# Optimization experiments

Measured on AMD Instinct MI355X. Metric: run time of the kernel, lower is better.

Reference implementation:

```python
import jax, jax.numpy as jnp
import numpy as np

B, X, H = 2048, 1024, 1024
DR = 0.5

def setup_inputs() -> dict:
    key = jax.random.key(0)
    ks = jax.random.split(key, 21)
    std = 1.0 / np.sqrt(H)
    u = lambda k, s: jax.random.uniform(k, s, jnp.float32, -std, std)
    bern = lambda k, s: (jax.random.bernoulli(k, 1.0 - DR, s) / (1.0 - DR)).astype(jnp.float32)
    return {
        "x": jax.random.normal(ks[0], (B, X), jnp.float32),
        "h0": jax.random.normal(ks[1], (B, H), jnp.float32),
        "c0": jax.random.normal(ks[2], (B, H), jnp.float32),
        "w_xi": u(ks[3], (H, X)), "w_xf": u(ks[4], (H, X)),
        "w_xc": u(ks[5], (H, X)), "w_xo": u(ks[6], (H, X)),
        "w_hi": u(ks[7], (H, H)), "w_hf": u(ks[8], (H, H)),
        "w_hc": u(ks[9], (H, H)), "w_ho": u(ks[10], (H, H)),
        "b_i": u(ks[11], (H,)), "b_f": u(ks[12], (H,)),
        "b_c": u(ks[13], (H,)), "b_o": u(ks[14], (H,)),
        "maskHI": bern(ks[15], (B, H)), "maskHF": bern(ks[16], (B, H)),
        "maskHC": bern(ks[17], (B, H)), "maskHO": bern(ks[18], (B, H)),
        "maskC": bern(ks[19], (B, H)),
    }

def reference(x, h0, c0,
              w_xi, w_xf, w_xc, w_xo,
              w_hi, w_hf, w_hc, w_ho,
              b_i, b_f, b_c, b_o,
              maskHI, maskHF, maskHC, maskHO, maskC):
    # gal dropout: per-gate masks on recurrent input h0
    hs = jnp.stack([h0 * maskHI, h0 * maskHF, h0 * maskHC, h0 * maskHO])  # [4,B,H]
    wh = jnp.stack([w_hi, w_hf, w_hc, w_ho])                              # [4,H,H]
    wx = jnp.stack([w_xi, w_xf, w_xc, w_xo])                              # [4,H,X]
    # two batched GEMMs (F.linear uses x @ W.T)
    g = jnp.einsum('bx,gkx->gbk', x, wx) + jnp.einsum('gbh,gkh->gbk', hs, wh)
    gateI = jax.nn.sigmoid(g[0] + b_i)
    gateF = jax.nn.sigmoid(g[1] + b_f)
    gateC = jnp.tanh(g[2] + b_c) * maskC   # sem dropout on candidate
    gateO = jax.nn.sigmoid(g[3] + b_o)
    c1 = gateF * c0 + gateI * gateC
    h1 = gateO * jnp.tanh(c1)
    return (h1, c1)
```

## Files before the change

### kernel.cpp

```cpp
#include <hip/hip_runtime.h>
#include <hip/hip_bf16.h>
#include <stdint.h>

#define BDIM 2048
#define HDIM 1024
#define XDIM 1024
#define BH (BDIM*HDIM)
#define WSEG 1048576

typedef __attribute__((ext_vector_type(8))) short short8;
typedef __attribute__((ext_vector_type(4))) float float4v;

__device__ __forceinline__ void gload16(const void* g, void* l) {
    __builtin_amdgcn_global_load_lds(
        (const __attribute__((address_space(1))) unsigned int*)g,
        (__attribute__((address_space(3))) unsigned int*)l, 16, 0, 0);
}

__device__ __forceinline__ unsigned pack2(float a, float b) {
    __hip_bfloat162 v = __float22bfloat162_rn(make_float2(a, b));
    return *reinterpret_cast<unsigned*>(&v);
}
__device__ __forceinline__ uint2 pack4(float4 f) {
    return make_uint2(pack2(f.x, f.y), pack2(f.z, f.w));
}
__device__ __forceinline__ float2 up2(unsigned u) {
    __hip_bfloat162 v = *reinterpret_cast<__hip_bfloat162*>(&u);
    return __bfloat1622float2(v);
}

__global__ __launch_bounds__(256) void prep_all_k(
    const float* __restrict__ w0, const float* __restrict__ w1,
    const float* __restrict__ w2, const float* __restrict__ w3,
    const float* __restrict__ w4, const float* __restrict__ w5,
    const float* __restrict__ w6, const float* __restrict__ w7,
    const float* __restrict__ x, const float* __restrict__ h0,
    const float* __restrict__ mI, const float* __restrict__ mF,
    const float* __restrict__ mC, const float* __restrict__ mO,
    uint2* __restrict__ dst) {
    const int seg = blockIdx.y;
    const int i = blockIdx.x * 256 + threadIdx.x;
    float4 f;
    if (seg < 10) {
        const float* base;
        switch (seg) {
            case 0: base = w0; break; case 1: base = w1; break;
            case 2: base = w2; break; case 3: base = w3; break;
            case 4: base = w4; break; case 5: base = w5; break;
            case 6: base = w6; break; case 7: base = w7; break;
            default: base = x + (size_t)(seg - 8) * WSEG; break;
        }
        f = ((const float4*)base)[i];
    } else {
        const int s = seg - 10;
        const int g = s >> 1, half = s & 1;
        const float* mp = (g == 0) ? mI : (g == 1) ? mF : (g == 2) ? mC : mO;
        float4 h = ((const float4*)(h0 + (size_t)half * WSEG))[i];
        float4 m = ((const float4*)(mp + (size_t)half * WSEG))[i];
        f = make_float4(h.x * m.x, h.y * m.y, h.z * m.z, h.w * m.w);
    }
    dst[(size_t)seg * (WSEG / 4) + i] = pack4(f);
}

__global__ __launch_bounds__(256, 4) void gemm_split(
    const __hip_bfloat16* __restrict__ ws18,
    __hip_bfloat16* __restrict__ part) {
    const int id = blockIdx.x;
    const int z = id & 7;
    const int by = (id >> 3) & 7;
    const int bx = id >> 6;
    const int g = z >> 1, half = z & 1;
    const __hip_bfloat16* Ap = half ? (ws18 + (size_t)(10 + 2 * g) * WSEG)
                                    : (ws18 + (size_t)8 * WSEG);
    const __hip_bfloat16* Bp = half ? (ws18 + (size_t)(4 + g) * WSEG)
                                    : (ws18 + (size_t)g * WSEG);

    __shared__ __hip_bfloat16 As[128 * 64];
    __shared__ __hip_bfloat16 Bs[128 * 64];

    const int t = threadIdx.x;
    const int m0 = bx * 128;
    const int n0 = by * 128;
    const int wv = t >> 6, lane = t & 63;
    const int wm = (wv >> 1) * 64, wn = (wv & 1) * 64;
    const int quad = lane >> 4, lrow = lane & 15;

    float4v acc[4][4];
#pragma unroll
    for (int i = 0; i < 4; ++i)
#pragma unroll
        for (int j = 0; j < 4; ++j) acc[i][j] = (float4v){0.f, 0.f, 0.f, 0.f};

    const short8* As8 = (const short8*)As;
    const short8* Bs8 = (const short8*)Bs;

    for (int k0 = 0; k0 < 1024; k0 += 64) {
#pragma unroll
        for (int it = 0; it < 4; ++it) {
            int chunk = it * 256 + t;
            int row = chunk >> 3;
            int ccs = (chunk & 7) ^ (row & 7);
            gload16(Ap + (size_t)(m0 + row) * 1024 + k0 + ccs * 8,
                    (char*)As + chunk * 16);
            gload16(Bp + (size_t)(n0 + row) * 1024 + k0 + ccs * 8,
                    (char*)Bs + chunk * 16);
        }
        __syncthreads();

#pragma unroll
        for (int ks = 0; ks < 2; ++ks) {
            short8 af[4], bfr[4];
#pragma unroll
            for (int mt = 0; mt < 4; ++mt) {
                int r = wm + mt * 16 + lrow;
                af[mt] = As8[(r << 3) + ((ks * 4 + quad) ^ (r & 7))];
            }
#pragma unroll
            for (int nt = 0; nt < 4; ++nt) {
                int r = wn + nt * 16 + lrow;
                bfr[nt] = Bs8[(r << 3) + ((ks * 4 + quad) ^ (r & 7))];
            }
#pragma unroll
            for (int mt = 0; mt < 4; ++mt)
#pragma unroll
                for (int nt = 0; nt < 4; ++nt)
                    acc[mt][nt] = __builtin_amdgcn_mfma_f32_16x16x32_bf16(
                        af[mt], bfr[nt], acc[mt][nt], 0, 0, 0);
        }
        __syncthreads();
    }

    __hip_bfloat16* pz = part + (size_t)z * BH;
#pragma unroll
    for (int nt = 0; nt < 4; ++nt) {
        int col = n0 + wn + nt * 16 + lrow;
#pragma unroll
        for (int mt = 0; mt < 4; ++mt) {
#pragma unroll
            for (int r = 0; r < 4; ++r) {
                int row = m0 + wm + mt * 16 + quad * 4 + r;
                pz[(size_t)row * HDIM + col] = __float2bfloat16(acc[mt][nt][r]);
            }
        }
    }
}

__global__ __launch_bounds__(256) void combine_k(
    const uint2* __restrict__ part,
    const float* __restrict__ bi, const float* __restrict__ bff,
    const float* __restrict__ bc, const float* __restrict__ bo,
    const float* __restrict__ c0, const float* __restrict__ mC,
    float4* __restrict__ out) {
    const int i = blockIdx.x * 256 + threadIdx.x;
    const int h4 = (i * 4 & (HDIM - 1)) >> 2;

    float gate[4][4];
#pragma unroll
    for (int g = 0; g < 4; ++g) {
        uint2 p0 = part[(size_t)(2 * g) * (BH / 4) + i];
        uint2 p1 = part[(size_t)(2 * g + 1) * (BH / 4) + i];
        float2 a0 = up2(p0.x), a1 = up2(p0.y);
        float2 b0 = up2(p1.x), b1 = up2(p1.y);
        gate[g][0] = a0.x + b0.x;
        gate[g][1] = a0.y + b0.y;
        gate[g][2] = a1.x + b1.x;
        gate[g][3] = a1.y + b1.y;
    }
    float4 vbi = ((const float4*)bi)[h4];
    float4 vbf = ((const float4*)bff)[h4];
    float4 vbc = ((const float4*)bc)[h4];
    float4 vbo = ((const float4*)bo)[h4];
    float4 vc0 = ((const float4*)c0)[i];
    float4 vmc = ((const float4*)mC)[i];
    const float* pbi = (const float*)&vbi;
    const float* pbf = (const float*)&vbf;
    const float* pbc = (const float*)&vbc;
    const float* pbo = (const float*)&vbo;
    const float* pc0 = (const float*)&vc0;
    const float* pmc = (const float*)&vmc;

    float h1[4], c1[4];
#pragma unroll
    for (int j = 0; j < 4; ++j) {
        float xi = gate[0][j] + pbi[j];
        float xf = gate[1][j] + pbf[j];
        float xc = gate[2][j] + pbc[j];
        float xo = gate[3][j] + pbo[j];
        float I = 1.f / (1.f + __expf(-xi));
        float F = 1.f / (1.f + __expf(-xf));
        float C = tanhf(xc) * pmc[j];
        float O = 1.f / (1.f + __expf(-xo));
        c1[j] = F * pc0[j] + I * C;
        h1[j] = O * tanhf(c1[j]);
    }
    out[i] = make_float4(h1[0], h1[1], h1[2], h1[3]);
    out[BH / 4 + i] = make_float4(c1[0], c1[1], c1[2], c1[3]);
}

extern "C" void kernel_launch(void* const* d_in, const int* in_sizes, int n_in,
                              void* d_out, int out_size, void* d_ws, size_t ws_size,
                              hipStream_t stream) {
    const float* x   = (const float*)d_in[0];
    const float* h0  = (const float*)d_in[1];
    const float* c0  = (const float*)d_in[2];
    const float* wxi = (const float*)d_in[3];
    const float* wxf = (const float*)d_in[4];
    const float* wxc = (const float*)d_in[5];
    const float* wxo = (const float*)d_in[6];
    const float* whi = (const float*)d_in[7];
    const float* whf = (const float*)d_in[8];
    const float* whc = (const float*)d_in[9];
    const float* who = (const float*)d_in[10];
    const float* bi  = (const float*)d_in[11];
    const float* bf  = (const float*)d_in[12];
    const float* bc  = (const float*)d_in[13];
    const float* bo  = (const float*)d_in[14];
    const float* mI  = (const float*)d_in[15];
    const float* mF  = (const float*)d_in[16];
    const float* mC  = (const float*)d_in[17];
    const float* mO  = (const float*)d_in[18];
    const float* mCell = (const float*)d_in[19];

    __hip_bfloat16* ws18 = (__hip_bfloat16*)d_ws;
    __hip_bfloat16* part = ws18 + (size_t)18 * WSEG;

    prep_all_k<<<dim3(WSEG / 4 / 256, 18), dim3(256), 0, stream>>>(
        wxi, wxf, wxc, wxo, whi, whf, whc, who, x, h0, mI, mF, mC, mO,
        (uint2*)ws18);

    gemm_split<<<dim3(1024), dim3(256), 0, stream>>>(ws18, part);

    combine_k<<<dim3(BH / 4 / 256), dim3(256), 0, stream>>>(
        (const uint2*)part, bi, bf, bc, bo, c0, mCell, (float4*)d_out);
}
```

Measured before the change: 202.9 us.

## Rewrite GEMM as 256x256-tile double-buffered pipeline with interleaved loads and MFMA

The split GEMM moves from 128x128 tiles with 256 threads and a single LDS buffer to 256x256 tiles with 512 threads (8 waves, each computing 128x64). LDS is double-buffered at 128 KB, and global-to-LDS loads for the next k-tile are issued in quarter slices between MFMA groups. Raw s_barrier, explicit vmcnt waits and setprio hints are used to overlap memory traffic with compute. This aims to raise operand reuse and hide load latency, at the cost of only 256 blocks on the device and much higher register and LDS pressure per block.

Result: no change. 200.6 us (-1.1%).

```diff
diff --git a/kernel.cpp b/kernel.cpp
--- a/kernel.cpp
+++ b/kernel.cpp
@@ -62,85 +62,177 @@
     dst[(size_t)seg * (WSEG / 4) + i] = pack4(f);
 }
 
-__global__ __launch_bounds__(256, 4) void gemm_split(
+
+#define BARRIER() asm volatile("s_barrier" ::: "memory")
+
+__device__ __forceinline__ void stage_half(const __hip_bfloat16* __restrict__ gp,
+                                           short* lb, int t) {
+    const int r0 = t >> 3;
+    const int c0 = (t & 7) ^ (r0 & 7);
+    gload16(gp + (size_t)r0 * 1024 + c0 * 8, (char*)lb + t * 16);
+    const int r1 = r0 + 64;
+    const int c1 = (t & 7) ^ (r1 & 7);
+    gload16(gp + (size_t)r1 * 1024 + c1 * 8, (char*)lb + t * 16 + 8192);
+}
+
+template<int P>
+__device__ __forceinline__ void read_bf(const short8* L8, int wn_i, int lrow, int quad,
+                                        short8 (&bfr)[4][2]) {
+    const int bb8 = 4096 + P * 2048 + (wn_i >> 1) * 1024;
+#pragma unroll
+    for (int nt = 0; nt < 4; ++nt) {
+        const int rb = (wn_i & 1) * 64 + nt * 16 + lrow;
+#pragma unroll
+        for (int ks = 0; ks < 2; ++ks)
+            bfr[nt][ks] = L8[bb8 + (rb << 3) + ((ks * 4 + quad) ^ (rb & 7))];
+    }
+}
+
+template<int P, int Q>
+__device__ __forceinline__ void read_af(const short8* L8, int wm_i, int lrow, int quad,
+                                        short8 (&af)[2][2]) {
+    const int ab8 = P * 2048 + wm_i * 1024;
+#pragma unroll
+    for (int sub = 0; sub < 2; ++sub) {
+        const int ra = Q * 32 + sub * 16 + lrow;
+#pragma unroll
+        for (int ks = 0; ks < 2; ++ks)
+            af[sub][ks] = L8[ab8 + (ra << 3) + ((ks * 4 + quad) ^ (ra & 7))];
+    }
+}
+
+template<int Q>
+__device__ __forceinline__ void mfma_q(short8 (&af)[2][2], short8 (&bfr)[4][2],
+                                       float4v (&acc)[8][4]) {
+    __builtin_amdgcn_s_setprio(1);
+#pragma unroll
+    for (int sub = 0; sub < 2; ++sub)
+#pragma unroll
+        for (int nt = 0; nt < 4; ++nt)
+#pragma unroll
+            for (int ks = 0; ks < 2; ++ks)
+                acc[2 * Q + sub][nt] = __builtin_amdgcn_mfma_f32_16x16x32_bf16(
+                    af[sub][ks], bfr[nt][ks], acc[2 * Q + sub][nt], 0, 0, 0);
+    __builtin_amdgcn_s_setprio(0);
+}
+
+__global__ __launch_bounds__(512, 2) void gemm_split(
     const __hip_bfloat16* __restrict__ ws18,
     __hip_bfloat16* __restrict__ part) {
     const int id = blockIdx.x;
     const int z = id & 7;
-    const int by = (id >> 3) & 7;
-    const int bx = id >> 6;
+    const int w = id >> 3;
+    const int by = w & 3;
+    const int bx = w >> 2;
     const int g = z >> 1, half = z & 1;
     const __hip_bfloat16* Ap = half ? (ws18 + (size_t)(10 + 2 * g) * WSEG)
                                     : (ws18 + (size_t)8 * WSEG);
     const __hip_bfloat16* Bp = half ? (ws18 + (size_t)(4 + g) * WSEG)
                                     : (ws18 + (size_t)g * WSEG);
 
-    __shared__ __hip_bfloat16 As[128 * 64];
-    __shared__ __hip_bfloat16 Bs[128 * 64];
+    __shared__ short lds[65536];
 
     const int t = threadIdx.x;
-    const int m0 = bx * 128;
-    const int n0 = by * 128;
-    const int wv = t >> 6, lane = t & 63;
-    const int wm = (wv >> 1) * 64, wn = (wv & 1) * 64;
-    const int quad = lane >> 4, lrow = lane & 15;
-
-    float4v acc[4][4];
-#pragma unroll
-    for (int i = 0; i < 4; ++i)
+    const int m0 = bx * 256, n0 = by * 256;
+    const int wid = t >> 6, lane = t & 63;
+    const int wm_i = wid >> 2, wn_i = wid & 3;
+    const int lrow = lane & 15, quad = lane >> 4;
+    const short8* L8 = (const short8*)lds;
+
+    float4v acc[8][4];
+#pragma unroll
+    for (int i = 0; i < 8; ++i)
 #pragma unroll
         for (int j = 0; j < 4; ++j) acc[i][j] = (float4v){0.f, 0.f, 0.f, 0.f};
 
-    const short8* As8 = (const short8*)As;
-    const short8* Bs8 = (const short8*)Bs;
-
-    for (int k0 = 0; k0 < 1024; k0 += 64) {
-#pragma unroll
-        for (int it = 0; it < 4; ++it) {
-            int chunk = it * 256 + t;
-            int row = chunk >> 3;
-            int ccs = (chunk & 7) ^ (row & 7);
-            gload16(Ap + (size_t)(m0 + row) * 1024 + k0 + ccs * 8,
-                    (char*)As + chunk * 16);
-            gload16(Bp + (size_t)(n0 + row) * 1024 + k0 + ccs * 8,
-                    (char*)Bs + chunk * 16);
+    auto stageA = [&](int k, int h) {
+        stage_half(Ap + (size_t)(m0 + h * 128) * 1024 + (size_t)k * 64,
+                   lds + (k & 1) * 16384 + h * 8192, t);
+    };
+    auto stageB = [&](int k, int h) {
+        stage_half(Bp + (size_t)(n0 + h * 128) * 1024 + (size_t)k * 64,
+                   lds + 32768 + (k & 1) * 16384 + h * 8192, t);
+    };
+
+    stageA(0, 0); stageA(0, 1); stageB(0, 0); stageB(0, 1); stageB(1, 0); stageB(1, 1);
+    asm volatile("s_waitcnt vmcnt(4)" ::: "memory");
+    BARRIER();
+
+    auto iter_body = [&](int i, bool last) {
+        const int T1 = 2 * i + 1;
+        short8 bfr[4][2];
+        short8 af[2][2];
+
+        read_bf<0>(L8, wn_i, lrow, quad, bfr);
+        read_af<0, 0>(L8, wm_i, lrow, quad, af);
+        stageA(T1, 0);
+        BARRIER(); __builtin_amdgcn_sched_barrier(0);
+        mfma_q<0>(af, bfr, acc);
+        BARRIER();
+
+        read_af<0, 1>(L8, wm_i, lrow, quad, af);
+        stageA(T1, 1);
+        BARRIER(); __builtin_amdgcn_sched_barrier(0);
+        mfma_q<1>(af, bfr, acc);
+        BARRIER();
+
+        read_af<0, 2>(L8, wm_i, lrow, quad, af);
+        if (!last) stageB(T1 + 1, 0);
+        BARRIER(); __builtin_amdgcn_sched_barrier(0);
+        mfma_q<2>(af, bfr, acc);
+        BARRIER();
+
+        read_af<0, 3>(L8, wm_i, lrow, quad, af);
+        if (!last) stageB(T1 + 1, 1);
+        BARRIER(); __builtin_amdgcn_sched_barrier(0);
+        mfma_q<3>(af, bfr, acc);
+        if (last) asm volatile("s_waitcnt vmcnt(0)" ::: "memory");
+        else      asm volatile("s_waitcnt vmcnt(4)" ::: "memory");
+        BARRIER();
+
+        read_bf<1>(L8, wn_i, lrow, quad, bfr);
+        read_af<1, 0>(L8, wm_i, lrow, quad, af);
+        if (!last) stageA(T1 + 1, 0);
+        BARRIER(); __builtin_amdgcn_sched_barrier(0);
+        mfma_q<0>(af, bfr, acc);
+        BARRIER();
+
+        read_af<1, 1>(L8, wm_i, lrow, quad, af);
+        if (!last) stageA(T1 + 1, 1);
+        BARRIER(); __builtin_amdgcn_sched_barrier(0);
+        mfma_q<1>(af, bfr, acc);
+        BARRIER();
+
+        read_af<1, 2>(L8, wm_i, lrow, quad, af);
+        if (!last) stageB(T1 + 2, 0);
+        BARRIER(); __builtin_amdgcn_sched_barrier(0);
+        mfma_q<2>(af, bfr, acc);
+        BARRIER();
+
+        read_af<1, 3>(L8, wm_i, lrow, quad, af);
+        if (!last) stageB(T1 + 2, 1);
+        BARRIER(); __builtin_amdgcn_sched_barrier(0);
+        mfma_q<3>(af, bfr, acc);
+        if (!last) {
+            asm volatile("s_waitcnt vmcnt(4)" ::: "memory");
+            BARRIER();
         }
-        __syncthreads();
-
-#pragma unroll
-        for (int ks = 0; ks < 2; ++ks) {
-            short8 af[4], bfr[4];
-#pragma unroll
-            for (int mt = 0; mt < 4; ++mt) {
-                int r = wm + mt * 16 + lrow;
-                af[mt] = As8[(r << 3) + ((ks * 4 + quad) ^ (r & 7))];
-            }
-#pragma unroll
-            for (int nt = 0; nt < 4; ++nt) {
-                int r = wn + nt * 16 + lrow;
-                bfr[nt] = Bs8[(r << 3) + ((ks * 4 + quad) ^ (r & 7))];
-            }
-#pragma unroll
-            for (int mt = 0; mt < 4; ++mt)
-#pragma unroll
-                for (int nt = 0; nt < 4; ++nt)
-                    acc[mt][nt] = __builtin_amdgcn_mfma_f32_16x16x32_bf16(
-                        af[mt], bfr[nt], acc[mt][nt], 0, 0, 0);
-        }
-        __syncthreads();
-    }
+    };
+
+#pragma unroll 1
+    for (int i = 0; i < 7; ++i) iter_body(i, false);
+    iter_body(7, true);
 
     __hip_bfloat16* pz = part + (size_t)z * BH;
 #pragma unroll
-    for (int nt = 0; nt < 4; ++nt) {
-        int col = n0 + wn + nt * 16 + lrow;
-#pragma unroll
-        for (int mt = 0; mt < 4; ++mt) {
-#pragma unroll
-            for (int r = 0; r < 4; ++r) {
-                int row = m0 + wm + mt * 16 + quad * 4 + r;
-                pz[(size_t)row * HDIM + col] = __float2bfloat16(acc[mt][nt][r]);
-            }
+    for (int mt = 0; mt < 8; ++mt) {
+        const int rowb = m0 + wm_i * 128 + mt * 16 + quad * 4;
+#pragma unroll
+        for (int nt = 0; nt < 4; ++nt) {
+            const int col = n0 + wn_i * 64 + nt * 16 + lrow;
+#pragma unroll
+            for (int r = 0; r < 4; ++r)
+                pz[(size_t)(rowb + r) * HDIM + col] = __float2bfloat16(acc[mt][nt][r]);
         }
     }
 }
@@ -228,7 +320,7 @@
         wxi, wxf, wxc, wxo, whi, whf, whc, who, x, h0, mI, mF, mC, mO,
         (uint2*)ws18);
 
-    gemm_split<<<dim3(1024), dim3(256), 0, stream>>>(ws18, part);
+    gemm_split<<<dim3(256), dim3(512), 0, stream>>>(ws18, part);
 
     combine_k<<<dim3(BH / 4 / 256), dim3(256), 0, stream>>>(
         (const uint2*)part, bi, bf, bc, bo, c0, mCell, (float4*)d_out);
```

## Enlarge GEMM tiles to 256x256 with double-buffered LDS prefetch

Applied to the files above, without the earlier changes.

The split GEMM now uses 512-thread blocks computing 256x256 output tiles, with each wave holding a 128x64 sub-tile. It double-buffers the 64-wide K slices in 128 KB of LDS, issuing the next slice's global-to-LDS loads before computing the current one and using one barrier per iteration. This is meant to cut global traffic per FLOP and hide load latency behind MFMA work. In exchange the grid shrinks to 256 blocks, which may leave compute units idle, and LDS and register pressure rise, limiting occupancy.

Result: no change. 203.8 us (+0.4%).

```diff
diff --git a/kernel.cpp b/kernel.cpp
--- a/kernel.cpp
+++ b/kernel.cpp
@@ -62,85 +62,101 @@
     dst[(size_t)seg * (WSEG / 4) + i] = pack4(f);
 }
 
-__global__ __launch_bounds__(256, 4) void gemm_split(
+
+#define BARRIER() asm volatile("s_barrier" ::: "memory")
+
+__global__ __launch_bounds__(512, 2) void gemm_split(
     const __hip_bfloat16* __restrict__ ws18,
     __hip_bfloat16* __restrict__ part) {
     const int id = blockIdx.x;
     const int z = id & 7;
-    const int by = (id >> 3) & 7;
-    const int bx = id >> 6;
+    const int w = id >> 3;
+    const int by = w & 3;
+    const int bx = w >> 2;
     const int g = z >> 1, half = z & 1;
     const __hip_bfloat16* Ap = half ? (ws18 + (size_t)(10 + 2 * g) * WSEG)
                                     : (ws18 + (size_t)8 * WSEG);
     const __hip_bfloat16* Bp = half ? (ws18 + (size_t)(4 + g) * WSEG)
                                     : (ws18 + (size_t)g * WSEG);
 
-    __shared__ __hip_bfloat16 As[128 * 64];
-    __shared__ __hip_bfloat16 Bs[128 * 64];
+    __shared__ short lds[65536];
 
     const int t = threadIdx.x;
-    const int m0 = bx * 128;
-    const int n0 = by * 128;
-    const int wv = t >> 6, lane = t & 63;
-    const int wm = (wv >> 1) * 64, wn = (wv & 1) * 64;
-    const int quad = lane >> 4, lrow = lane & 15;
-
-    float4v acc[4][4];
-#pragma unroll
-    for (int i = 0; i < 4; ++i)
+    const int m0 = bx * 256, n0 = by * 256;
+    const int wid = t >> 6, lane = t & 63;
+    const int wm_i = wid >> 2, wn_i = wid & 3;
+    const int lrow = lane & 15, quad = lane >> 4;
+    const short8* L8 = (const short8*)lds;
+
+    float4v acc[8][4];
+#pragma unroll
+    for (int i = 0; i < 8; ++i)
 #pragma unroll
         for (int j = 0; j < 4; ++j) acc[i][j] = (float4v){0.f, 0.f, 0.f, 0.f};
 
-    const short8* As8 = (const short8*)As;
-    const short8* Bs8 = (const short8*)Bs;
-
-    for (int k0 = 0; k0 < 1024; k0 += 64) {
+    auto stage = [&](int k) {
+        const int bufB = (k & 1) * 32768;
+        const int kc = k * 64;
 #pragma unroll
         for (int it = 0; it < 4; ++it) {
-            int chunk = it * 256 + t;
-            int row = chunk >> 3;
-            int ccs = (chunk & 7) ^ (row & 7);
-            gload16(Ap + (size_t)(m0 + row) * 1024 + k0 + ccs * 8,
-                    (char*)As + chunk * 16);
-            gload16(Bp + (size_t)(n0 + row) * 1024 + k0 + ccs * 8,
-                    (char*)Bs + chunk * 16);
-        }
-        __syncthreads();
-
-#pragma unroll
-        for (int ks = 0; ks < 2; ++ks) {
-            short8 af[4], bfr[4];
-#pragma unroll
-            for (int mt = 0; mt < 4; ++mt) {
-                int r = wm + mt * 16 + lrow;
-                af[mt] = As8[(r << 3) + ((ks * 4 + quad) ^ (r & 7))];
+            const int c = it * 512 + t;
+            const int row = c >> 3;
+            const int cg = (c & 7) ^ (row & 7);
+            gload16(Ap + (size_t)(m0 + row) * 1024 + kc + cg * 8,
+                    (char*)lds + bufB + c * 16);
+            gload16(Bp + (size_t)(n0 + row) * 1024 + kc + cg * 8,
+                    (char*)lds + 65536 + bufB + c * 16);
+        }
+    };
+
+    auto compute = [&](int k) {
+        const int ab = (k & 1) * 2048;
+        const int bb = 4096 + ab;
+        short8 bfr[4][2];
+#pragma unroll
+        for (int nt = 0; nt < 4; ++nt) {
+            const int rb = wn_i * 64 + nt * 16 + lrow;
+#pragma unroll
+            for (int ks = 0; ks < 2; ++ks)
+                bfr[nt][ks] = L8[bb + (rb << 3) + ((ks * 4 + quad) ^ (rb & 7))];
+        }
+#pragma unroll
+        for (int mt = 0; mt < 8; ++mt) {
+            const int ra = wm_i * 128 + mt * 16 + lrow;
+            short8 a0 = L8[ab + (ra << 3) + (quad ^ (ra & 7))];
+            short8 a1 = L8[ab + (ra << 3) + ((4 + quad) ^ (ra & 7))];
+#pragma unroll
+            for (int nt = 0; nt < 4; ++nt) {
+                acc[mt][nt] = __builtin_amdgcn_mfma_f32_16x16x32_bf16(
+                    a0, bfr[nt][0], acc[mt][nt], 0, 0, 0);
+                acc[mt][nt] = __builtin_amdgcn_mfma_f32_16x16x32_bf16(
+                    a1, bfr[nt][1], acc[mt][nt], 0, 0, 0);
             }
-#pragma unroll
-            for (int nt = 0; nt < 4; ++nt) {
-                int r = wn + nt * 16 + lrow;
-                bfr[nt] = Bs8[(r << 3) + ((ks * 4 + quad) ^ (r & 7))];
-            }
-#pragma unroll
-            for (int mt = 0; mt < 4; ++mt)
-#pragma unroll
-                for (int nt = 0; nt < 4; ++nt)
-                    acc[mt][nt] = __builtin_amdgcn_mfma_f32_16x16x32_bf16(
-                        af[mt], bfr[nt], acc[mt][nt], 0, 0, 0);
-        }
-        __syncthreads();
+        }
+    };
+
+    stage(0);
+    asm volatile("s_waitcnt vmcnt(0)" ::: "memory");
+    BARRIER();
+
+#pragma unroll 1
+    for (int k = 0; k < 16; ++k) {
+        if (k < 15) stage(k + 1);
+        compute(k);
+        asm volatile("s_waitcnt vmcnt(0)" ::: "memory");
+        BARRIER();
     }
 
     __hip_bfloat16* pz = part + (size_t)z * BH;
 #pragma unroll
-    for (int nt = 0; nt < 4; ++nt) {
-        int col = n0 + wn + nt * 16 + lrow;
-#pragma unroll
-        for (int mt = 0; mt < 4; ++mt) {
-#pragma unroll
-            for (int r = 0; r < 4; ++r) {
-                int row = m0 + wm + mt * 16 + quad * 4 + r;
-                pz[(size_t)row * HDIM + col] = __float2bfloat16(acc[mt][nt][r]);
-            }
+    for (int mt = 0; mt < 8; ++mt) {
+        const int rowb = m0 + wm_i * 128 + mt * 16 + quad * 4;
+#pragma unroll
+        for (int nt = 0; nt < 4; ++nt) {
+            const int col = n0 + wn_i * 64 + nt * 16 + lrow;
+#pragma unroll
+            for (int r = 0; r < 4; ++r)
+                pz[(size_t)(rowb + r) * HDIM + col] = __float2bfloat16(acc[mt][nt][r]);
         }
     }
 }
@@ -228,7 +244,7 @@
         wxi, wxf, wxc, wxo, whi, whf, whc, who, x, h0, mI, mF, mC, mO,
         (uint2*)ws18);
 
-    gemm_split<<<dim3(1024), dim3(256), 0, stream>>>(ws18, part);
+    gemm_split<<<dim3(256), dim3(512), 0, stream>>>(ws18, part);
 
     combine_k<<<dim3(BH / 4 / 256), dim3(256), 0, stream>>>(
         (const uint2*)part, bi, bf, bc, bo, c0, mCell, (float4*)d_out);
```
